# Optimization experiments

Measured on AMD Instinct MI355X. Metric: run time of the kernel, lower is better.

The kernel has to match this reference:

```python
import jax, jax.numpy as jnp
import numpy as np

# static config (matches init_kwargs)
C, NH, WS, H, W, NQ, PS = 384, 12, 8, 56, 56, 64, 8
HD = C // NH
SCALE = HD ** -0.5
EPS = 1e-5
MLP_H = 4 * C


def _rel_pos_index():
    ch, cw = np.meshgrid(np.arange(WS), np.arange(WS), indexing='ij')
    cf = np.stack([ch.ravel(), cw.ravel()])                      # [2, WS*WS]
    rel = cf[:, :, None] - cf[:, None, :]                        # [2, N, N]
    rel = rel.transpose(1, 2, 0)
    rel[:, :, 0] += WS - 1
    rel[:, :, 1] += WS - 1
    rel[:, :, 0] *= 2 * WS - 1
    return jnp.asarray(rel.sum(-1))                              # [N, N] int

REL_IDX = _rel_pos_index()


def _ln(x, g, b):
    mu = x.mean(-1, keepdims=True)
    var = ((x - mu) ** 2).mean(-1, keepdims=True)
    return (x - mu) * jax.lax.rsqrt(var + EPS) * g + b


def setup_inputs() -> dict:
    key = jax.random.key(0)
    ks = jax.random.split(key, 24)
    B = 16
    n = lambda k, shp, s=0.02: jax.random.normal(k, shp, dtype=jnp.float32) * s
    inp = {
        'x': jax.random.normal(ks[0], (B, H * W, C), dtype=jnp.float32),
        'query_tokens': n(ks[1], (1, NQ, C)),
        'kproj_w': n(ks[2], (C, C)), 'kproj_b': jnp.zeros((C,)),
        'kbn_g': jnp.ones((C,)), 'kbn_b': jnp.zeros((C,)),
        'vproj_w': n(ks[3], (C, C)), 'vproj_b': jnp.zeros((C,)),
        'vbn_g': jnp.ones((C,)), 'vbn_b': jnp.zeros((C,)),
        'ck_w': n(ks[4], (C, C)), 'ck_b': jnp.zeros((C,)),
        'cv_w': n(ks[5], (C, C)), 'cv_b': jnp.zeros((C,)),
        'qkv_w': n(ks[6], (C, 3 * C)), 'qkv_b': jnp.zeros((3 * C,)),
        'proj_w': n(ks[7], (C, C)), 'proj_b': jnp.zeros((C,)),
        'rpb_table': n(ks[8], ((2 * WS - 1) ** 2, NH)),
        'norm1_g': jnp.ones((C,)), 'norm1_b': jnp.zeros((C,)),
        'norm2_g': jnp.ones((C,)), 'norm2_b': jnp.zeros((C,)),
        'fc1_w': n(ks[9], (C, MLP_H)), 'fc1_b': jnp.zeros((MLP_H,)),
        'fc2_w': n(ks[10], (MLP_H, C)), 'fc2_b': jnp.zeros((C,)),
    }
    return inp


def _forward(x, query_tokens, kproj_w, kproj_b, kbn_g, kbn_b, vproj_w, vproj_b,
             vbn_g, vbn_b, ck_w, ck_b, cv_w, cv_b, qkv_w, qkv_b, proj_w, proj_b,
             rpb_table, norm1_g, norm1_b, norm2_g, norm2_b, fc1_w, fc1_b, fc2_w, fc2_b):
    B, L, _ = x.shape
    shortcut = x
    xn = _ln(x, norm1_g, norm1_b)                                # [B, L, C]

    # ---- global cross attention (pooled tokens -> learnable queries) ----
    x4 = xn.reshape(B, H, W, C)
    pooled = x4.reshape(B, H // PS, PS, W // PS, PS, C).mean(axis=(2, 4))  # [B,7,7,C]
    pooled = pooled.reshape(B, (H // PS) * (W // PS), C)         # [B, 49, C]
    # conv1x1 + BatchNorm2d (eval mode, default running stats mean=0, var=1)
    bn_scale = 1.0 / jnp.sqrt(1.0 + EPS)
    key = ((pooled @ kproj_w + kproj_b) * bn_scale) * kbn_g + kbn_b
    val = ((pooled @ vproj_w + vproj_b) * bn_scale) * vbn_g + vbn_b

    q = jnp.broadcast_to(query_tokens, (B, NQ, C))
    qh = q.reshape(B, NQ, NH, HD).transpose(0, 2, 1, 3)          # [B,NH,NQ,HD]
    kh = key.reshape(B, -1, NH, HD).transpose(0, 2, 1, 3)
    vh = val.reshape(B, -1, NH, HD).transpose(0, 2, 1, 3)
    attn = jax.nn.softmax(jnp.einsum('bhqd,bhkd->bhqk', qh, kh) * SCALE, axis=-1)
    o = jnp.einsum('bhqk,bhkd->bhqd', attn, vh).transpose(0, 2, 1, 3).reshape(B, NQ, C)
    gk = (o + q) @ ck_w + ck_b                                   # [B, NQ, C]
    gv = (o + q) @ cv_w + cv_b

    # ---- windowed attention with global kv concat ----
    nW = (H // WS) * (W // WS)
    N = WS * WS
    xw = (x4.reshape(B, H // WS, WS, W // WS, WS, C)
             .transpose(0, 1, 3, 2, 4, 5)
             .reshape(B * nW, N, C))                             # [B_, N, C]
    qkv = (xw @ qkv_w + qkv_b).reshape(B * nW, N, 3, NH, HD).transpose(2, 0, 3, 1, 4)
    wq, wk, wv = qkv[0], qkv[1], qkv[2]                          # [B_, NH, N, HD]

    gkh = jnp.broadcast_to(gk.reshape(B, 1, NQ, NH, HD), (B, nW, NQ, NH, HD))
    gkh = gkh.reshape(B * nW, NQ, NH, HD).transpose(0, 2, 1, 3)  # [B_, NH, NQ, HD]
    gvh = jnp.broadcast_to(gv.reshape(B, 1, NQ, NH, HD), (B, nW, NQ, NH, HD))
    gvh = gvh.reshape(B * nW, NQ, NH, HD).transpose(0, 2, 1, 3)
    wk = jnp.concatenate([wk, gkh], axis=2)                      # [B_, NH, N+NQ, HD]
    wv = jnp.concatenate([wv, gvh], axis=2)

    logits = jnp.einsum('bhqd,bhkd->bhqk', wq * SCALE, wk)       # [B_, NH, N, N+NQ]
    rpb = rpb_table[REL_IDX.reshape(-1)].reshape(N, N, NH).transpose(2, 0, 1)  # [NH,N,N]
    logits = logits.at[:, :, :, :N].add(rpb[None])
    wattn = jax.nn.softmax(logits, axis=-1)
    ow = jnp.einsum('bhqk,bhkd->bhqd', wattn, wv).transpose(0, 2, 1, 3).reshape(B * nW, N, C)
    ow = ow @ proj_w + proj_b

    # window reverse
    xr = (ow.reshape(B, H // WS, W // WS, WS, WS, C)
             .transpose(0, 1, 3, 2, 4, 5)
             .reshape(B, H * W, C))

    x = shortcut + xr
    h = jax.nn.gelu(_ln(x, norm2_g, norm2_b) @ fc1_w + fc1_b, approximate=False)
    return x + (h @ fc2_w + fc2_b)


def reference(x, query_tokens, kproj_w, kproj_b, kbn_g, kbn_b, vproj_w, vproj_b,
              vbn_g, vbn_b, ck_w, ck_b, cv_w, cv_b, qkv_w, qkv_b, proj_w, proj_b,
              rpb_table, norm1_g, norm1_b, norm2_g, norm2_b, fc1_w, fc1_b, fc2_w, fc2_b):
    return _forward(x, query_tokens, kproj_w, kproj_b, kbn_g, kbn_b, vproj_w, vproj_b,
                    vbn_g, vbn_b, ck_w, ck_b, cv_w, cv_b, qkv_w, qkv_b, proj_w, proj_b,
                    rpb_table, norm1_g, norm1_b, norm2_g, norm2_b, fc1_w, fc1_b, fc2_w, fc2_b)
```

## Files before the change

kernel.cpp:

```cpp
#include <hip/hip_runtime.h>
#include <math.h>

typedef __attribute__((ext_vector_type(8))) __bf16 bf16x8;
typedef __attribute__((ext_vector_type(4))) float f32x4;
typedef __attribute__((ext_vector_type(8))) unsigned short u16x8;

#define DI __device__ __forceinline__

DI float b2f(unsigned short u) { return __uint_as_float(((unsigned int)u) << 16); }
DI unsigned short f2b(float f) {
    unsigned int x = __float_as_uint(f);
    x += 0x7fffu + ((x >> 16) & 1u);
    return (unsigned short)(x >> 16);
}
DI unsigned short f2b_fast(float f) {
    __bf16 h = (__bf16)f;
    return *(unsigned short*)&h;
}

DI void gl16(const unsigned short* g, unsigned short* l) {
    __builtin_amdgcn_global_load_lds(
        (const __attribute__((address_space(1))) void*)g,
        (__attribute__((address_space(3))) void*)l,
        16, 0, 0);
}

#define SCALE_ATT 0.17677669529663687f
#define BN_SCALE  0.9999950000374997f

__global__ __launch_bounds__(256) void cvt_t_kernel(const float* __restrict__ in,
                                                    unsigned short* __restrict__ out,
                                                    int Kd, int Nd) {
    int i = blockIdx.x * 256 + threadIdx.x;
    if (i < Kd * Nd) {
        int k = i / Nd, n = i % Nd;
        out[(size_t)n * Kd + k] = f2b(in[i]);
    }
}

__global__ __launch_bounds__(64) void ln_kernel(const float* __restrict__ xin,
                                                const float* __restrict__ g,
                                                const float* __restrict__ bsh,
                                                unsigned short* __restrict__ out) {
    int row = blockIdx.x;
    int t = threadIdx.x;
    size_t base = (size_t)row * 384;
    float v[6];
    float s = 0.f;
#pragma unroll
    for (int p = 0; p < 6; ++p) { v[p] = xin[base + t + 64 * p]; s += v[p]; }
#pragma unroll
    for (int off = 32; off > 0; off >>= 1) s += __shfl_xor(s, off);
    float mu = s * (1.f / 384.f);
    float q = 0.f;
#pragma unroll
    for (int p = 0; p < 6; ++p) { float d = v[p] - mu; q += d * d; }
#pragma unroll
    for (int off = 32; off > 0; off >>= 1) q += __shfl_xor(q, off);
    float rstd = rsqrtf(q * (1.f / 384.f) + 1e-5f);
#pragma unroll
    for (int p = 0; p < 6; ++p) {
        int c = t + 64 * p;
        out[base + c] = f2b((v[p] - mu) * rstd * g[c] + bsh[c]);
    }
}

__global__ __launch_bounds__(384) void pool_kernel(const unsigned short* __restrict__ xn,
                                                   float* __restrict__ pooled) {
    int blk = blockIdx.x;
    int b = blk / 49, pp = blk % 49;
    int ph = pp / 7, pw = pp % 7;
    int c = threadIdx.x;
    float s = 0.f;
    for (int i = 0; i < 8; ++i) {
        size_t rb = ((size_t)b * 3136 + (size_t)(ph * 8 + i) * 56 + pw * 8) * 384;
        for (int j = 0; j < 8; ++j) s += b2f(xn[rb + (size_t)j * 384 + c]);
    }
    pooled[(size_t)blk * 384 + c] = s * (1.f / 64.f);
}

__global__ __launch_bounds__(128) void kvproj_kernel(
    const float* __restrict__ pooled,
    const float* __restrict__ kw, const float* __restrict__ kb,
    const float* __restrict__ kg, const float* __restrict__ kbb,
    const float* __restrict__ vw, const float* __restrict__ vb,
    const float* __restrict__ vg, const float* __restrict__ vbb,
    float* __restrict__ keyo, float* __restrict__ valo) {
    __shared__ float row[384];
    int r = blockIdx.x;
    int t = threadIdx.x;
    for (int c = t; c < 384; c += 128) row[c] = pooled[(size_t)r * 384 + c];
    __syncthreads();
#pragma unroll
    for (int p = 0; p < 3; ++p) {
        int c = t + 128 * p;
        float aK = 0.f, aV = 0.f;
        for (int k = 0; k < 384; ++k) {
            float rv = row[k];
            aK += rv * kw[(size_t)k * 384 + c];
            aV += rv * vw[(size_t)k * 384 + c];
        }
        keyo[(size_t)r * 384 + c] = (aK + kb[c]) * BN_SCALE * kg[c] + kbb[c];
        valo[(size_t)r * 384 + c] = (aV + vb[c]) * BN_SCALE * vg[c] + vbb[c];
    }
}

__global__ __launch_bounds__(64) void rpb_expand_kernel(const float* __restrict__ rpbt,
                                                        float* __restrict__ rpb_mat) {
    int h = blockIdx.x >> 6, q = blockIdx.x & 63;
    int k = threadIdx.x;
    int i1 = q >> 3, j1 = q & 7, i2 = k >> 3, j2 = k & 7;
    rpb_mat[((size_t)h * 64 + q) * 64 + k] = rpbt[(size_t)((i1 - i2 + 7) * 15 + (j1 - j2 + 7)) * 12 + h];
}

__global__ __launch_bounds__(64) void cross_attn_kernel(const float* __restrict__ keyg,
                                                        const float* __restrict__ valg,
                                                        const float* __restrict__ qtok,
                                                        float* __restrict__ o) {
    int b = blockIdx.x / 12, h = blockIdx.x % 12;
    __shared__ float kk[49][32];
    __shared__ float vv[49][32];
    int t = threadIdx.x;
    for (int idx = t; idx < 49 * 32; idx += 64) {
        int k = idx >> 5, d = idx & 31;
        size_t gidx = ((size_t)b * 49 + k) * 384 + h * 32 + d;
        kk[k][d] = keyg[gidx];
        vv[k][d] = valg[gidx];
    }
    __syncthreads();
    float q[32];
#pragma unroll
    for (int d = 0; d < 32; ++d) q[d] = qtok[(size_t)t * 384 + h * 32 + d] * SCALE_ATT;
    float lg[49];
    float mx = -1e30f;
#pragma unroll
    for (int k = 0; k < 49; ++k) {
        float s = 0.f;
#pragma unroll
        for (int d = 0; d < 32; ++d) s += q[d] * kk[k][d];
        lg[k] = s;
        mx = fmaxf(mx, s);
    }
    float sum = 0.f;
#pragma unroll
    for (int k = 0; k < 49; ++k) { float e = expf(lg[k] - mx); lg[k] = e; sum += e; }
    float inv = 1.f / sum;
    float od[32];
#pragma unroll
    for (int d = 0; d < 32; ++d) od[d] = 0.f;
#pragma unroll
    for (int k = 0; k < 49; ++k) {
        float wgt = lg[k];
#pragma unroll
        for (int d = 0; d < 32; ++d) od[d] += wgt * vv[k][d];
    }
#pragma unroll
    for (int d = 0; d < 32; ++d) o[((size_t)b * 64 + t) * 384 + h * 32 + d] = od[d] * inv;
}

__global__ __launch_bounds__(128) void gkv_kernel(
    const float* __restrict__ o, const float* __restrict__ qtok,
    const float* __restrict__ ckw, const float* __restrict__ ckb,
    const float* __restrict__ cvw, const float* __restrict__ cvb,
    unsigned short* __restrict__ gk, unsigned short* __restrict__ gv) {
    __shared__ float row[384];
    int r = blockIdx.x;
    int n = r & 63;
    int t = threadIdx.x;
    for (int c = t; c < 384; c += 128)
        row[c] = o[(size_t)r * 384 + c] + qtok[(size_t)n * 384 + c];
    __syncthreads();
#pragma unroll
    for (int p = 0; p < 3; ++p) {
        int c = t + 128 * p;
        float aK = 0.f, aV = 0.f;
        for (int k = 0; k < 384; ++k) {
            float rv = row[k];
            aK += rv * ckw[(size_t)k * 384 + c];
            aV += rv * cvw[(size_t)k * 384 + c];
        }
        gk[(size_t)r * 384 + c] = f2b(aK + ckb[c]);
        gv[(size_t)r * 384 + c] = f2b(aV + cvb[c]);
    }
}

template <int MODE>
__global__ __launch_bounds__(256) void gemm128(const unsigned short* __restrict__ A,
                                               const unsigned short* __restrict__ BT,
                                               const float* __restrict__ bias,
                                               int N, int K,
                                               void* __restrict__ outp,
                                               const void* __restrict__ aux0) {
    __shared__ __align__(16) unsigned short As[128 * 32];
    __shared__ __align__(16) unsigned short Bs[128 * 32];
    int bn = blockIdx.x, bm = blockIdx.y;
    int t = threadIdx.x;
    int w = t >> 6, lane = t & 63;
    int wm = w >> 1, wn = w & 1;
    int lo = lane & 15, g = lane >> 4;

    f32x4 acc[4][4];
#pragma unroll
    for (int i = 0; i < 4; ++i)
#pragma unroll
        for (int j = 0; j < 4; ++j) acc[i][j] = f32x4{0.f, 0.f, 0.f, 0.f};

    int srow = w * 32 + (lane >> 2);
    int schunk = (lane & 3) << 3;
    const unsigned short* Ap0 = A + (size_t)(bm * 128 + srow) * K + schunk;
    const unsigned short* Ap1 = A + (size_t)(bm * 128 + srow + 16) * K + schunk;
    const unsigned short* Bp0 = BT + (size_t)(bn * 128 + srow) * K + schunk;
    const unsigned short* Bp1 = BT + (size_t)(bn * 128 + srow + 16) * K + schunk;
    unsigned short* AsD0 = As + (w * 32) * 32;
    unsigned short* AsD1 = As + (w * 32 + 16) * 32;
    unsigned short* BsD0 = Bs + (w * 32) * 32;
    unsigned short* BsD1 = Bs + (w * 32 + 16) * 32;

    for (int kb = 0; kb < K; kb += 32) {
        gl16(Ap0 + kb, AsD0);
        gl16(Ap1 + kb, AsD1);
        gl16(Bp0 + kb, BsD0);
        gl16(Bp1 + kb, BsD1);
        __syncthreads();
        bf16x8 af[4], bfv[4];
#pragma unroll
        for (int m = 0; m < 4; ++m)
            af[m] = *(const bf16x8*)(As + (wm * 64 + m * 16 + lo) * 32 + g * 8);
#pragma unroll
        for (int n = 0; n < 4; ++n)
            bfv[n] = *(const bf16x8*)(Bs + (wn * 64 + n * 16 + lo) * 32 + g * 8);
#pragma unroll
        for (int m = 0; m < 4; ++m)
#pragma unroll
            for (int n = 0; n < 4; ++n)
                acc[m][n] = __builtin_amdgcn_mfma_f32_16x16x32_bf16(af[m], bfv[n], acc[m][n], 0, 0, 0);
        __syncthreads();
    }

    int r0 = bm * 128 + wm * 64 + g * 4;
    int c0 = bn * 128 + wn * 64 + lo;
#pragma unroll
    for (int m = 0; m < 4; ++m)
#pragma unroll
        for (int n = 0; n < 4; ++n)
#pragma unroll
            for (int j = 0; j < 4; ++j) {
                int r = r0 + m * 16 + j;
                int c = c0 + n * 16;
                float v = acc[m][n][j] + bias[c];
                if (MODE == 0) {
                    ((unsigned short*)outp)[(size_t)r * N + c] = f2b(v);
                } else if (MODE == 1) {
                    int wg = r >> 6, nn = r & 63;
                    int b = wg / 49, win = wg % 49;
                    int wh = win / 7, ww = win % 7;
                    int l = ((wh << 3) + (nn >> 3)) * 56 + (ww << 3) + (nn & 7);
                    size_t idx = ((size_t)b * 3136 + l) * 384 + c;
                    ((float*)outp)[idx] = ((const float*)aux0)[idx] + v;
                } else if (MODE == 2) {
                    float ge = 0.5f * v * (1.f + erff(v * 0.70710678118654752f));
                    ((unsigned short*)outp)[(size_t)r * N + c] = f2b(ge);
                } else {
                    float res = ((const float*)aux0)[(size_t)r * 384 + c];
                    ((float*)outp)[(size_t)r * N + c] = v + res;
                }
            }
}

__global__ __launch_bounds__(64, 2) void win_attn_mfma(const unsigned short* __restrict__ qkv,
                                                       const unsigned short* __restrict__ gkb,
                                                       const unsigned short* __restrict__ gvb,
                                                       const float* __restrict__ rpb_mat,
                                                       unsigned short* __restrict__ ow) {
    int blk = blockIdx.x;
    int wg = blk / 12, h = blk % 12;
    int b = wg / 49, win = wg % 49;
    int wh = win / 7, ww = win % 7;
    int lane = threadIdx.x;
    int lo = lane & 15, g = lane >> 4;

    __shared__ __align__(16) unsigned short VT[32 * 136];
    __shared__ __align__(16) unsigned short PL[64 * 40];

    size_t qkvbase = (size_t)b * 3136 * 1152;
    int lbase = ((wh << 3)) * 56 + (ww << 3);

    {
        int n = lane;
        int l = lbase + (n >> 3) * 56 + (n & 7);
        const unsigned short* vp = qkv + qkvbase + (size_t)l * 1152 + 768 + h * 32;
        u16x8 v0 = *(const u16x8*)(vp);
        u16x8 v1 = *(const u16x8*)(vp + 8);
        u16x8 v2 = *(const u16x8*)(vp + 16);
        u16x8 v3 = *(const u16x8*)(vp + 24);
#pragma unroll
        for (int j = 0; j < 8; ++j) {
            VT[(0 + j) * 136 + n]  = v0[j];
            VT[(8 + j) * 136 + n]  = v1[j];
            VT[(16 + j) * 136 + n] = v2[j];
            VT[(24 + j) * 136 + n] = v3[j];
        }
        const unsigned short* gp = gvb + ((size_t)b * 64 + n) * 384 + h * 32;
        v0 = *(const u16x8*)(gp);
        v1 = *(const u16x8*)(gp + 8);
        v2 = *(const u16x8*)(gp + 16);
        v3 = *(const u16x8*)(gp + 24);
#pragma unroll
        for (int j = 0; j < 8; ++j) {
            VT[(0 + j) * 136 + 64 + n]  = v0[j];
            VT[(8 + j) * 136 + 64 + n]  = v1[j];
            VT[(16 + j) * 136 + 64 + n] = v2[j];
            VT[(24 + j) * 136 + 64 + n] = v3[j];
        }
    }

    bf16x8 qf[4];
#pragma unroll
    for (int qt = 0; qt < 4; ++qt) {
        int n = qt * 16 + lo;
        int l = lbase + (n >> 3) * 56 + (n & 7);
        qf[qt] = *(const bf16x8*)(qkv + qkvbase + (size_t)l * 1152 + h * 32 + g * 8);
    }

    f32x4 S[4][8];
#pragma unroll
    for (int qt = 0; qt < 4; ++qt)
#pragma unroll
        for (int t = 0; t < 8; ++t) S[qt][t] = f32x4{0.f, 0.f, 0.f, 0.f};

#pragma unroll
    for (int t = 0; t < 8; ++t) {
        bf16x8 kf;
        if (t < 4) {
            int key = t * 16 + lo;
            int l = lbase + (key >> 3) * 56 + (key & 7);
            kf = *(const bf16x8*)(qkv + qkvbase + (size_t)l * 1152 + 384 + h * 32 + g * 8);
        } else {
            int gkey = (t - 4) * 16 + lo;
            kf = *(const bf16x8*)(gkb + ((size_t)b * 64 + gkey) * 384 + h * 32 + g * 8);
        }
#pragma unroll
        for (int qt = 0; qt < 4; ++qt)
            S[qt][t] = __builtin_amdgcn_mfma_f32_16x16x32_bf16(qf[qt], kf, S[qt][t], 0, 0, 0);
    }

    const float* rb_h = rpb_mat + (size_t)h * 4096;
    float mx[4][4];
#pragma unroll
    for (int qt = 0; qt < 4; ++qt)
#pragma unroll
        for (int j = 0; j < 4; ++j) mx[qt][j] = -1e30f;

#pragma unroll
    for (int qt = 0; qt < 4; ++qt) {
#pragma unroll
        for (int t = 0; t < 8; ++t) {
#pragma unroll
            for (int j = 0; j < 4; ++j) {
                float v = S[qt][t][j] * SCALE_ATT;
                if (t < 4) v += rb_h[(qt * 16 + g * 4 + j) * 64 + t * 16 + lo];
                S[qt][t][j] = v;
                mx[qt][j] = fmaxf(mx[qt][j], v);
            }
        }
    }
#pragma unroll
    for (int qt = 0; qt < 4; ++qt)
#pragma unroll
        for (int j = 0; j < 4; ++j) {
#pragma unroll
            for (int m = 1; m <= 8; m <<= 1)
                mx[qt][j] = fmaxf(mx[qt][j], __shfl_xor(mx[qt][j], m));
        }

    float sm[4][4];
#pragma unroll
    for (int qt = 0; qt < 4; ++qt)
#pragma unroll
        for (int j = 0; j < 4; ++j) sm[qt][j] = 0.f;
#pragma unroll
    for (int qt = 0; qt < 4; ++qt)
#pragma unroll
        for (int t = 0; t < 8; ++t)
#pragma unroll
            for (int j = 0; j < 4; ++j) {
                float p = __expf(S[qt][t][j] - mx[qt][j]);
                S[qt][t][j] = p;
                sm[qt][j] += p;
            }
#pragma unroll
    for (int qt = 0; qt < 4; ++qt)
#pragma unroll
        for (int j = 0; j < 4; ++j) {
#pragma unroll
            for (int m = 1; m <= 8; m <<= 1)
                sm[qt][j] += __shfl_xor(sm[qt][j], m);
        }
    float inv[4][4];
#pragma unroll
    for (int qt = 0; qt < 4; ++qt)
#pragma unroll
        for (int j = 0; j < 4; ++j) inv[qt][j] = 1.f / sm[qt][j];

    f32x4 O[4][2];
#pragma unroll
    for (int qt = 0; qt < 4; ++qt)
#pragma unroll
        for (int dt = 0; dt < 2; ++dt) O[qt][dt] = f32x4{0.f, 0.f, 0.f, 0.f};

#pragma unroll
    for (int c = 0; c < 4; ++c) {
        __syncthreads();
#pragma unroll
        for (int qt = 0; qt < 4; ++qt) {
            int qb = qt * 16 + g * 4;
#pragma unroll
            for (int half = 0; half < 2; ++half) {
                int t = 2 * c + half;
#pragma unroll
                for (int j = 0; j < 4; ++j)
                    PL[(qb + j) * 40 + half * 16 + lo] = f2b_fast(S[qt][t][j]);
            }
        }
        __syncthreads();
#pragma unroll
        for (int qt = 0; qt < 4; ++qt) {
            bf16x8 pa = *(const bf16x8*)(PL + (qt * 16 + lo) * 40 + g * 8);
#pragma unroll
            for (int dt = 0; dt < 2; ++dt) {
                bf16x8 vb = *(const bf16x8*)(VT + (dt * 16 + lo) * 136 + c * 32 + g * 8);
                O[qt][dt] = __builtin_amdgcn_mfma_f32_16x16x32_bf16(pa, vb, O[qt][dt], 0, 0, 0);
            }
        }
    }

#pragma unroll
    for (int qt = 0; qt < 4; ++qt)
#pragma unroll
        for (int dt = 0; dt < 2; ++dt)
#pragma unroll
            for (int j = 0; j < 4; ++j) {
                int q = qt * 16 + g * 4 + j;
                int d = dt * 16 + lo;
                ow[((size_t)wg * 64 + q) * 384 + h * 32 + d] = f2b_fast(O[qt][dt][j] * inv[qt][j]);
            }
}

static const size_t OFF_XN   = 0;
static const size_t OFF_QKV  = 38535168;
static const size_t OFF_OW   = 154140672;
static const size_t OFF_X2   = 192675840;
static const size_t OFF_PL   = 269746176;
static const size_t OFF_KEY  = 270950400;
static const size_t OFF_VAL  = 272154624;
static const size_t OFF_O    = 273358848;
static const size_t OFF_GK   = 274931712;
static const size_t OFF_GV   = 276504576;
static const size_t OFF_QKVW = 278077440;
static const size_t OFF_PRJW = 278962176;
static const size_t OFF_FC1W = 279257088;
static const size_t OFF_FC2W = 280436736;

extern "C" void kernel_launch(void* const* d_in, const int* in_sizes, int n_in,
                              void* d_out, int out_size, void* d_ws, size_t ws_size,
                              hipStream_t stream) {
    const float* x      = (const float*)d_in[0];
    const float* qtok   = (const float*)d_in[1];
    const float* kprojw = (const float*)d_in[2];
    const float* kprojb = (const float*)d_in[3];
    const float* kbng   = (const float*)d_in[4];
    const float* kbnb   = (const float*)d_in[5];
    const float* vprojw = (const float*)d_in[6];
    const float* vprojb = (const float*)d_in[7];
    const float* vbng   = (const float*)d_in[8];
    const float* vbnb   = (const float*)d_in[9];
    const float* ckw    = (const float*)d_in[10];
    const float* ckb    = (const float*)d_in[11];
    const float* cvw    = (const float*)d_in[12];
    const float* cvb    = (const float*)d_in[13];
    const float* qkvw   = (const float*)d_in[14];
    const float* qkvb   = (const float*)d_in[15];
    const float* projw  = (const float*)d_in[16];
    const float* projb  = (const float*)d_in[17];
    const float* rpbt   = (const float*)d_in[18];
    const float* n1g    = (const float*)d_in[19];
    const float* n1b    = (const float*)d_in[20];
    const float* n2g    = (const float*)d_in[21];
    const float* n2b    = (const float*)d_in[22];
    const float* fc1w   = (const float*)d_in[23];
    const float* fc1b   = (const float*)d_in[24];
    const float* fc2w   = (const float*)d_in[25];
    const float* fc2b   = (const float*)d_in[26];

    char* wsb = (char*)d_ws;
    unsigned short* xn     = (unsigned short*)(wsb + OFF_XN);
    unsigned short* qkvbf  = (unsigned short*)(wsb + OFF_QKV);
    unsigned short* owbf   = (unsigned short*)(wsb + OFF_OW);
    float* x2      = (float*)(wsb + OFF_X2);
    float* pooled  = (float*)(wsb + OFF_PL);
    float* rpb_mat = (float*)(wsb + OFF_PL);
    float* keyg    = (float*)(wsb + OFF_KEY);
    float* valg    = (float*)(wsb + OFF_VAL);
    float* obuf    = (float*)(wsb + OFF_O);
    unsigned short* gkb = (unsigned short*)(wsb + OFF_GK);
    unsigned short* gvb = (unsigned short*)(wsb + OFF_GV);
    unsigned short* qkvw_t = (unsigned short*)(wsb + OFF_QKVW);
    unsigned short* prjw_t = (unsigned short*)(wsb + OFF_PRJW);
    unsigned short* fc1w_t = (unsigned short*)(wsb + OFF_FC1W);
    unsigned short* fc2w_t = (unsigned short*)(wsb + OFF_FC2W);
    unsigned short* ln2out = (unsigned short*)(wsb + OFF_XN);
    unsigned short* hbuf   = (unsigned short*)(wsb + OFF_QKV);

    cvt_t_kernel<<<(442368 + 255) / 256, 256, 0, stream>>>(qkvw, qkvw_t, 384, 1152);
    cvt_t_kernel<<<(147456 + 255) / 256, 256, 0, stream>>>(projw, prjw_t, 384, 384);
    cvt_t_kernel<<<(589824 + 255) / 256, 256, 0, stream>>>(fc1w, fc1w_t, 384, 1536);
    cvt_t_kernel<<<(589824 + 255) / 256, 256, 0, stream>>>(fc2w, fc2w_t, 1536, 384);
    ln_kernel<<<50176, 64, 0, stream>>>(x, n1g, n1b, xn);
    pool_kernel<<<784, 384, 0, stream>>>(xn, pooled);
    kvproj_kernel<<<784, 128, 0, stream>>>(pooled, kprojw, kprojb, kbng, kbnb,
                                           vprojw, vprojb, vbng, vbnb, keyg, valg);
    rpb_expand_kernel<<<768, 64, 0, stream>>>(rpbt, rpb_mat);
    cross_attn_kernel<<<192, 64, 0, stream>>>(keyg, valg, qtok, obuf);
    gkv_kernel<<<1024, 128, 0, stream>>>(obuf, qtok, ckw, ckb, cvw, cvb, gkb, gvb);
    gemm128<0><<<dim3(9, 392), 256, 0, stream>>>(xn, qkvw_t, qkvb, 1152, 384, qkvbf, nullptr);
    win_attn_mfma<<<9408, 64, 0, stream>>>(qkvbf, gkb, gvb, rpb_mat, owbf);
    gemm128<1><<<dim3(3, 392), 256, 0, stream>>>(owbf, prjw_t, projb, 384, 384, x2, x);
    ln_kernel<<<50176, 64, 0, stream>>>(x2, n2g, n2b, ln2out);
    gemm128<2><<<dim3(12, 392), 256, 0, stream>>>(ln2out, fc1w_t, fc1b, 1536, 384, hbuf, nullptr);
    gemm128<3><<<dim3(3, 392), 256, 0, stream>>>(hbuf, fc2w_t, fc2b, 384, 1536, (float*)d_out, x2);
}
```

Measured before the change: 814.4 us.

## Double-buffer GEMM LDS tiles, swizzle block order, use tanh GELU

The 128x128 bf16 GEMM now keeps two LDS buffers, so the global-to-LDS loads for the next K tile overlap the MFMA work on the current one, with one barrier per tile instead of two. Workgroup indices are remapped in an interleaved order to change L2 reuse and traffic across the GPU. The exact erf GELU in the fc1 epilogue is replaced by the tanh approximation built on __expf. This differs from the reference's exact GELU and adds a small numerical error, and the doubled LDS use may lower occupancy. The block remap also assumes the workgroup count divides by 8.

```diff
diff --git a/kernel.cpp b/kernel.cpp
--- a/kernel.cpp
+++ b/kernel.cpp
@@ -23,6 +23,14 @@
         (const __attribute__((address_space(1))) void*)g,
         (__attribute__((address_space(3))) void*)l,
         16, 0, 0);
+}
+
+DI float gelu_f(float v) {
+    float u = v * (0.7978845608f + 0.0356774081f * v * v);
+    u = fminf(fmaxf(u, -15.f), 15.f);
+    float e = __expf(2.f * u);
+    float th = (e - 1.f) / (e + 1.f);
+    return 0.5f * v * (1.f + th);
 }
 
 #define SCALE_ATT 0.17677669529663687f
@@ -191,9 +199,14 @@
                                                int N, int K,
                                                void* __restrict__ outp,
                                                const void* __restrict__ aux0) {
-    __shared__ __align__(16) unsigned short As[128 * 32];
-    __shared__ __align__(16) unsigned short Bs[128 * 32];
-    int bn = blockIdx.x, bm = blockIdx.y;
+    __shared__ __align__(16) unsigned short As[2][128 * 32];
+    __shared__ __align__(16) unsigned short Bs[2][128 * 32];
+
+    int nwg = gridDim.x * gridDim.y;
+    int flat = blockIdx.y * gridDim.x + blockIdx.x;
+    int flat2 = (flat & 7) * (nwg >> 3) + (flat >> 3);
+    int bn = flat2 % gridDim.x, bm = flat2 / gridDim.x;
+
     int t = threadIdx.x;
     int w = t >> 6, lane = t & 63;
     int wm = w >> 1, wn = w & 1;
@@ -211,31 +224,58 @@
     const unsigned short* Ap1 = A + (size_t)(bm * 128 + srow + 16) * K + schunk;
     const unsigned short* Bp0 = BT + (size_t)(bn * 128 + srow) * K + schunk;
     const unsigned short* Bp1 = BT + (size_t)(bn * 128 + srow + 16) * K + schunk;
-    unsigned short* AsD0 = As + (w * 32) * 32;
-    unsigned short* AsD1 = As + (w * 32 + 16) * 32;
-    unsigned short* BsD0 = Bs + (w * 32) * 32;
-    unsigned short* BsD1 = Bs + (w * 32 + 16) * 32;
-
-    for (int kb = 0; kb < K; kb += 32) {
-        gl16(Ap0 + kb, AsD0);
-        gl16(Ap1 + kb, AsD1);
-        gl16(Bp0 + kb, BsD0);
-        gl16(Bp1 + kb, BsD1);
-        __syncthreads();
-        bf16x8 af[4], bfv[4];
-#pragma unroll
-        for (int m = 0; m < 4; ++m)
-            af[m] = *(const bf16x8*)(As + (wm * 64 + m * 16 + lo) * 32 + g * 8);
-#pragma unroll
-        for (int n = 0; n < 4; ++n)
-            bfv[n] = *(const bf16x8*)(Bs + (wn * 64 + n * 16 + lo) * 32 + g * 8);
-#pragma unroll
-        for (int m = 0; m < 4; ++m)
-#pragma unroll
-            for (int n = 0; n < 4; ++n)
-                acc[m][n] = __builtin_amdgcn_mfma_f32_16x16x32_bf16(af[m], bfv[n], acc[m][n], 0, 0, 0);
-        __syncthreads();
-    }
+    int d0 = (w * 32) * 32, d1 = (w * 32 + 16) * 32;
+
+#define STAGE(buf, kb)                    \
+    do {                                  \
+        gl16(Ap0 + (kb), As[buf] + d0);   \
+        gl16(Ap1 + (kb), As[buf] + d1);   \
+        gl16(Bp0 + (kb), Bs[buf] + d0);   \
+        gl16(Bp1 + (kb), Bs[buf] + d1);   \
+    } while (0)
+
+#define WAITBAR()                                          \
+    do {                                                   \
+        asm volatile("s_waitcnt vmcnt(0)" ::: "memory");   \
+        __builtin_amdgcn_s_barrier();                      \
+    } while (0)
+
+#define COMPUTE(buf)                                                                     \
+    do {                                                                                 \
+        bf16x8 af[4], bfv[4];                                                            \
+        _Pragma("unroll")                                                                \
+        for (int m = 0; m < 4; ++m)                                                      \
+            af[m] = *(const bf16x8*)(As[buf] + (wm * 64 + m * 16 + lo) * 32 + g * 8);    \
+        _Pragma("unroll")                                                                \
+        for (int n = 0; n < 4; ++n)                                                      \
+            bfv[n] = *(const bf16x8*)(Bs[buf] + (wn * 64 + n * 16 + lo) * 32 + g * 8);   \
+        _Pragma("unroll")                                                                \
+        for (int m = 0; m < 4; ++m)                                                      \
+            _Pragma("unroll")                                                            \
+            for (int n = 0; n < 4; ++n)                                                  \
+                acc[m][n] = __builtin_amdgcn_mfma_f32_16x16x32_bf16(af[m], bfv[n],       \
+                                                                    acc[m][n], 0, 0, 0); \
+    } while (0)
+
+    STAGE(0, 0);
+    WAITBAR();
+
+    int nt = K >> 5;
+    for (int tt = 0; tt < nt; tt += 2) {
+        STAGE(1, (tt + 1) * 32);
+        COMPUTE(0);
+        WAITBAR();
+        if (tt + 2 < nt) {
+            STAGE(0, (tt + 2) * 32);
+            COMPUTE(1);
+            WAITBAR();
+        } else {
+            COMPUTE(1);
+        }
+    }
+#undef STAGE
+#undef WAITBAR
+#undef COMPUTE
 
     int r0 = bm * 128 + wm * 64 + g * 4;
     int c0 = bn * 128 + wn * 64 + lo;
@@ -258,8 +298,7 @@
                     size_t idx = ((size_t)b * 3136 + l) * 384 + c;
                     ((float*)outp)[idx] = ((const float*)aux0)[idx] + v;
                 } else if (MODE == 2) {
-                    float ge = 0.5f * v * (1.f + erff(v * 0.70710678118654752f));
-                    ((unsigned short*)outp)[(size_t)r * N + c] = f2b(ge);
+                    ((unsigned short*)outp)[(size_t)r * N + c] = f2b(gelu_f(v));
                 } else {
                     float res = ((const float*)aux0)[(size_t)r * 384 + c];
                     ((float*)outp)[(size_t)r * N + c] = v + res;
```

After: 823.3 us. No clear change (+1.1%).
